# Kernel tuning notes

Hardware: AMD Instinct MI355X
Metric: run time of the kernel (lower is better)

The kernel has to match this reference:

```python
import jax, jax.numpy as jnp
import numpy as np

B, L, D, V, C = 16384, 50, 128, 91718, 11
H, HD, F = 4, 32, 6
NP = F * (F - 1) // 2  # 15 pairs
CIN = F * D + NP * D   # 2688


def setup_inputs() -> dict:
    key = jax.random.key(0)
    ks = jax.random.split(key, 32)
    inp = {}
    inp['item_id'] = jax.random.randint(ks[0], (B,), 0, V)
    inp['item_mm'] = jax.random.normal(ks[1], (B, D), dtype=jnp.float32)
    inp['likes'] = jax.random.randint(ks[2], (B,), 0, C)
    inp['views'] = jax.random.randint(ks[3], (B,), 0, C)
    inp['item_seq'] = jax.random.randint(ks[4], (B, L), 0, V)
    g = lambda k, shape, s: (jax.random.normal(k, shape, dtype=jnp.float32) * s)
    inp['item_emb'] = g(ks[5], (V, D), 0.02).at[0].set(0.0)  # padding_idx=0
    inp['cate_emb'] = g(ks[6], (C, D), 0.02)
    inp['mm_w'] = g(ks[7], (D, D), (2.0 / D) ** 0.5)
    inp['mm_b'] = jnp.zeros((D,), jnp.float32)
    inp['ln_g'] = jnp.ones((D,), jnp.float32)
    inp['ln_b'] = jnp.zeros((D,), jnp.float32)
    inp['gnn_W'] = g(ks[8], (H, D, HD), (2.0 / (D + HD)) ** 0.5 * 1.414)
    inp['gnn_a'] = g(ks[9], (H, 2 * HD, 1), 0.1)
    inp['se_w1'] = g(ks[10], (F, F // 2), 0.4)
    inp['se_b1'] = jnp.zeros((F // 2,), jnp.float32)
    inp['se_w2'] = g(ks[11], (F // 2, F), 0.4)
    inp['se_b2'] = jnp.zeros((F,), jnp.float32)
    inp['bi_W'] = g(ks[12], (F - 1, D, D), (2.0 / (2 * D)) ** 0.5)
    inp['mlp_w1'] = g(ks[13], (CIN, 512), (2.0 / CIN) ** 0.5)
    inp['mlp_b1'] = jnp.zeros((512,), jnp.float32)
    inp['bn1_g'] = jnp.ones((512,), jnp.float32)
    inp['bn1_b'] = jnp.zeros((512,), jnp.float32)
    inp['mlp_w2'] = g(ks[14], (512, 256), (2.0 / 512) ** 0.5)
    inp['mlp_b2'] = jnp.zeros((256,), jnp.float32)
    inp['bn2_g'] = jnp.ones((256,), jnp.float32)
    inp['bn2_b'] = jnp.zeros((256,), jnp.float32)
    inp['mlp_w3'] = g(ks[15], (256, 1), (2.0 / 256) ** 0.5)
    inp['mlp_b3'] = jnp.zeros((1,), jnp.float32)
    return inp


def _forward(item_id, item_mm, likes, views, item_seq,
             item_emb, cate_emb, mm_w, mm_b, ln_g, ln_b,
             gnn_W, gnn_a, se_w1, se_b1, se_w2, se_b2, bi_W,
             mlp_w1, mlp_b1, bn1_g, bn1_b, mlp_w2, mlp_b2, bn2_g, bn2_b,
             mlp_w3, mlp_b3):
    bsz = item_id.shape[0]
    eps = 1e-5

    user_feat = jnp.zeros((bsz, D), item_mm.dtype)
    like_feat = cate_emb[likes]
    view_feat = cate_emb[views]
    id_feat = item_emb[item_id]

    # mm_proj: Linear -> LayerNorm -> GELU (exact)
    y = item_mm @ mm_w + mm_b
    mu = y.mean(-1, keepdims=True)
    var = y.var(-1, keepdims=True)
    y = (y - mu) * jax.lax.rsqrt(var + eps) * ln_g + ln_b
    img_feat = jax.nn.gelu(y, approximate=False)

    # masked mean pooling of history
    seq_emb = item_emb[item_seq]                          # [B,L,D]
    mask = item_seq == 0
    seq_emb = jnp.where(mask[..., None], 0.0, seq_emb)
    cnt = jnp.clip(jnp.sum((~mask).astype(seq_emb.dtype), axis=1, keepdims=True), 1.0)
    hist_feat = seq_emb.sum(1) / cnt

    x = jnp.stack([user_feat, like_feat, view_feat, id_feat, img_feat, hist_feat], axis=1)  # [B,6,D]

    # GAT over 6-node fully-connected feature graph
    hp = jnp.einsum('bni,hio->bnho', x, gnn_W)            # [B,6,H,HD]
    a1 = gnn_a[:, :HD, 0]                                  # [H,HD]
    a2 = gnn_a[:, HD:, 0]
    ei = jnp.einsum('bnhd,hd->bhn', hp, a1)
    ej = jnp.einsum('bnhd,hd->bhn', hp, a2)
    e = ei[:, :, :, None] + ej[:, :, None, :]             # [B,H,6,6]
    e = jnp.where(e > 0, e, 0.2 * e)                       # LeakyReLU(0.2)
    att = jax.nn.softmax(e, axis=-1)                       # dropout off (eval)
    h_new = jnp.einsum('bhnm,bmho->bnho', att, hp).reshape(bsz, F, D)
    gnn_feat = jax.nn.elu(h_new + x)                       # in_dim == out_dim

    # SENet
    z = gnn_feat.mean(-1)                                  # [B,6]
    w = jax.nn.sigmoid(jax.nn.relu(z @ se_w1 + se_b1) @ se_w2 + se_b2)
    s = gnn_feat * w[..., None]

    # Bilinear ('each'): vid_i = s_i @ W_i, pairs (i,j), j>i
    vid = jnp.einsum('bfd,fde->bfe', s[:, :F - 1], bi_W)   # [B,5,D]
    p = jnp.stack([vid[:, i] * s[:, j] for i in range(F - 1) for j in range(i + 1, F)], axis=1)  # [B,15,D]

    c = jnp.concatenate([gnn_feat.reshape(bsz, -1), p.reshape(bsz, -1)], axis=1)  # [B,2688]

    # MLP with eval-mode BatchNorm (running mean 0, var 1) and dropout off
    bn = lambda t, g_, b_: t * (g_ / jnp.sqrt(1.0 + eps)) + b_
    h1 = jax.nn.gelu(bn(c @ mlp_w1 + mlp_b1, bn1_g, bn1_b), approximate=False)
    h2 = jax.nn.gelu(bn(h1 @ mlp_w2 + mlp_b2, bn2_g, bn2_b), approximate=False)
    out = jax.nn.sigmoid(h2 @ mlp_w3 + mlp_b3)
    return out.squeeze(-1)


def reference(item_id, item_mm, likes, views, item_seq,
              item_emb, cate_emb, mm_w, mm_b, ln_g, ln_b,
              gnn_W, gnn_a, se_w1, se_b1, se_w2, se_b2, bi_W,
              mlp_w1, mlp_b1, bn1_g, bn1_b, mlp_w2, mlp_b2, bn2_g, bn2_b,
              mlp_w3, mlp_b3):
    return _forward(item_id, item_mm, likes, views, item_seq,
                    item_emb, cate_emb, mm_w, mm_b, ln_g, ln_b,
                    gnn_W, gnn_a, se_w1, se_b1, se_w2, se_b2, bi_W,
                    mlp_w1, mlp_b1, bn1_g, bn1_b, mlp_w2, mlp_b2, bn2_g, bn2_b,
                    mlp_w3, mlp_b3)
```

## Files before the change

kernel.cpp:

```cpp
#include <hip/hip_runtime.h>
#include <hip/hip_bf16.h>
#include <cstdint>
#include <cstddef>

#define BB 16384

typedef float  floatx4 __attribute__((ext_vector_type(4)));
typedef float  floatx2 __attribute__((ext_vector_type(2)));
typedef __bf16 bf16x8  __attribute__((ext_vector_type(8)));

__device__ __forceinline__ unsigned short f2bf(float f) {
  union { float f; unsigned int u; } v; v.f = f;
  unsigned int r = v.u + 0x7FFFu + ((v.u >> 16) & 1u);
  return (unsigned short)(r >> 16);
}
__device__ __forceinline__ float bf2f(unsigned short h) {
  union { unsigned int u; float f; } v; v.u = ((unsigned int)h) << 16;
  return v.f;
}
__device__ __forceinline__ float gelu_exact(float x) {
  return 0.5f * x * (1.0f + erff(x * 0.7071067811865475f));
}
__device__ __forceinline__ void fp8x8_to_f32(uint2 v, float* o) {
  floatx2 p0 = __builtin_amdgcn_cvt_pk_f32_fp8((int)v.x, false);
  floatx2 p1 = __builtin_amdgcn_cvt_pk_f32_fp8((int)v.x, true);
  floatx2 p2 = __builtin_amdgcn_cvt_pk_f32_fp8((int)v.y, false);
  floatx2 p3 = __builtin_amdgcn_cvt_pk_f32_fp8((int)v.y, true);
  o[0] = p0.x; o[1] = p0.y; o[2] = p1.x; o[3] = p1.y;
  o[4] = p2.x; o[5] = p2.y; o[6] = p3.x; o[7] = p3.y;
}

#define ALOAD16(g, l) \
  __builtin_amdgcn_global_load_lds((const __attribute__((address_space(1))) void*)(g), \
                                   (__attribute__((address_space(3))) void*)(l), 16, 0, 0)

__global__ __launch_bounds__(256)
void k_prep(const float* __restrict__ gnn_W, const float* __restrict__ gnn_a,
            const float* __restrict__ item_mm, const float* __restrict__ item_emb,
            const float* __restrict__ w1, const float* __restrict__ w2,
            const float* __restrict__ bi_W, const float* __restrict__ mm_w,
            unsigned short* __restrict__ wallt2, unsigned short* __restrict__ immb,
            unsigned char* __restrict__ iembf8,
            unsigned short* __restrict__ w1t, unsigned short* __restrict__ w2t,
            unsigned short* __restrict__ biwt, unsigned short* __restrict__ mmwt)
{
  __shared__ float tile[64][65];
  if (blockIdx.x < 2048) {
    const int total = 18432 + 524288 + 1467488;
    for (int id = blockIdx.x * 256 + threadIdx.x; id < total; id += 2048 * 256) {
      if (id < 18432) {
        int n = id / 128, k = id % 128;
        if (n < 128) {
          wallt2[id] = f2bf(gnn_W[(n >> 5) * 4096 + k * 32 + (n & 31)]);
        } else if (n < 136) {
          int h = (n - 128) & 3;
          int off = (n < 132) ? 0 : 32;
          float s = 0.f;
          for (int o = 0; o < 32; o++)
            s += gnn_W[h * 4096 + k * 32 + o] * gnn_a[h * 64 + off + o];
          wallt2[id] = f2bf(s);
        } else {
          wallt2[id] = 0;
        }
      } else if (id < 542720) {
        int l = id - 18432;
        float4 v = ((const float4*)item_mm)[l];
        ushort4 o; o.x = f2bf(v.x); o.y = f2bf(v.y); o.z = f2bf(v.z); o.w = f2bf(v.w);
        ((ushort4*)immb)[l] = o;
      } else {
        int l = id - 542720;
        const float4 v0 = ((const float4*)item_emb)[l * 2];
        const float4 v1 = ((const float4*)item_emb)[l * 2 + 1];
        int lo = __builtin_amdgcn_cvt_pk_fp8_f32(v0.x, v0.y, 0, false);
        lo     = __builtin_amdgcn_cvt_pk_fp8_f32(v0.z, v0.w, lo, true);
        int hi = __builtin_amdgcn_cvt_pk_fp8_f32(v1.x, v1.y, 0, false);
        hi     = __builtin_amdgcn_cvt_pk_fp8_f32(v1.z, v1.w, hi, true);
        uint2 o; o.x = (unsigned int)lo; o.y = (unsigned int)hi;
        ((uint2*)iembf8)[l] = o;
      }
    }
  } else {
    int blk = blockIdx.x - 2048;
    const float* in; unsigned short* outp; int R, C, bx, by;
    if (blk < 336)      { in = w1; outp = w1t; R = 2688; C = 512; bx = blk % 8; by = blk / 8; }
    else if (blk < 368) { blk -= 336; in = w2; outp = w2t; R = 512; C = 256; bx = blk % 4; by = blk / 4; }
    else if (blk < 388) { blk -= 368; int f = blk / 4; int r2 = blk % 4;
                          in = bi_W + f * 16384; outp = biwt + f * 16384;
                          R = 128; C = 128; bx = r2 % 2; by = r2 / 2; }
    else                { blk -= 388; in = mm_w; outp = mmwt; R = 128; C = 128;
                          bx = blk % 2; by = blk / 2; }
    const int c0 = bx * 64, r0 = by * 64;
    const int lr = threadIdx.x >> 6;
    const int lc = threadIdx.x & 63;
    #pragma unroll
    for (int i = 0; i < 16; i++) {
      int r = lr + i * 4;
      tile[r][lc] = in[(size_t)(r0 + r) * C + c0 + lc];
    }
    __syncthreads();
    #pragma unroll
    for (int i = 0; i < 16; i++) {
      int c = lr + i * 4;
      outp[(size_t)(c0 + c) * R + r0 + lc] = f2bf(tile[lc][c]);
    }
  }
}

__global__ __launch_bounds__(512)
void k_featmm(const int* __restrict__ item_id, const int* __restrict__ likes,
              const int* __restrict__ views, const int* __restrict__ item_seq,
              const unsigned char* __restrict__ iembf8, const float* __restrict__ cate_emb,
              const unsigned short* __restrict__ immb, const unsigned short* __restrict__ mmwt,
              const float* __restrict__ mm_b, const float* __restrict__ ln_g,
              const float* __restrict__ ln_b, unsigned short* __restrict__ xb)
{
  __shared__ __align__(16) char smem[64 * 130 * 4];
  const int t = threadIdx.x, lane = t & 63, w = t >> 6;

  if (blockIdx.x < 2048) {
    const int b = blockIdx.x * 8 + w;
    const int g = lane >> 4, l16 = lane & 15;
    const size_t base = (size_t)b * 768;
    const int li = likes[b], vi = views[b], id = item_id[b];

    const int ng = (g < 2) ? 13 : 12;
    int idxs[13];
    #pragma unroll
    for (int e = 0; e < 13; e++)
      idxs[e] = (e < ng) ? item_seq[b * 50 + g + 4 * e] : 0;

    float acc[8] = {0.f, 0.f, 0.f, 0.f, 0.f, 0.f, 0.f, 0.f};
    float cnt = 0.f;
    #pragma unroll
    for (int e = 0; e < 13; e++) {
      const int idx = idxs[e];
      if (idx != 0) {
        cnt += 1.0f;
        uint2 v = *(const uint2*)&iembf8[(size_t)idx * 128 + l16 * 8];
        float dv[8];
        fp8x8_to_f32(v, dv);
        #pragma unroll
        for (int k = 0; k < 8; k++) acc[k] += dv[k];
      }
    }
    #pragma unroll
    for (int k = 0; k < 8; k++) {
      acc[k] += __shfl_xor(acc[k], 16, 64);
      acc[k] += __shfl_xor(acc[k], 32, 64);
    }
    cnt += __shfl_xor(cnt, 16, 64);
    cnt += __shfl_xor(cnt, 32, 64);
    const float ic = 1.0f / fmaxf(cnt, 1.0f);

    *(unsigned int*)&xb[base + lane * 2] = 0u;

    if (g == 0) {
      uint4 o;
      o.x = (unsigned int)f2bf(acc[0] * ic) | ((unsigned int)f2bf(acc[1] * ic) << 16);
      o.y = (unsigned int)f2bf(acc[2] * ic) | ((unsigned int)f2bf(acc[3] * ic) << 16);
      o.z = (unsigned int)f2bf(acc[4] * ic) | ((unsigned int)f2bf(acc[5] * ic) << 16);
      o.w = (unsigned int)f2bf(acc[6] * ic) | ((unsigned int)f2bf(acc[7] * ic) << 16);
      *(uint4*)&xb[base + 640 + l16 * 8] = o;
    } else if (g == 1) {
      uint2 v = *(const uint2*)&iembf8[(size_t)id * 128 + l16 * 8];
      float dv[8];
      fp8x8_to_f32(v, dv);
      uint4 o;
      o.x = (unsigned int)f2bf(dv[0]) | ((unsigned int)f2bf(dv[1]) << 16);
      o.y = (unsigned int)f2bf(dv[2]) | ((unsigned int)f2bf(dv[3]) << 16);
      o.z = (unsigned int)f2bf(dv[4]) | ((unsigned int)f2bf(dv[5]) << 16);
      o.w = (unsigned int)f2bf(dv[6]) | ((unsigned int)f2bf(dv[7]) << 16);
      *(uint4*)&xb[base + 384 + l16 * 8] = o;
    } else {
      const int ci = (g == 2) ? li : vi;
      const float4 v0 = *(const float4*)&cate_emb[(size_t)ci * 128 + l16 * 8];
      const float4 v1 = *(const float4*)&cate_emb[(size_t)ci * 128 + l16 * 8 + 4];
      uint4 o;
      o.x = (unsigned int)f2bf(v0.x) | ((unsigned int)f2bf(v0.y) << 16);
      o.y = (unsigned int)f2bf(v0.z) | ((unsigned int)f2bf(v0.w) << 16);
      o.z = (unsigned int)f2bf(v1.x) | ((unsigned int)f2bf(v1.y) << 16);
      o.w = (unsigned int)f2bf(v1.z) | ((unsigned int)f2bf(v1.w) << 16);
      *(uint4*)&xb[base + 128 + (g - 2) * 128 + l16 * 8] = o;
    }
    return;
  }

  unsigned short* As = (unsigned short*)smem;
  unsigned short* Bs = (unsigned short*)(smem + 8192);
  float* cls = (float*)smem;

  const int lr = lane & 15, lq = lane >> 4;
  const int m0 = (blockIdx.x - 2048) * 64;

  floatx4 acc[4];
  #pragma unroll
  for (int a = 0; a < 4; a++) acc[a] = (floatx4){0.f, 0.f, 0.f, 0.f};

  const int srow = lane >> 3;
  const int schk = (lane & 7) ^ srow;
  const int rb0 = w * 24;

  for (int k0 = 0; k0 < 128; k0 += 64) {
    __syncthreads();
    #pragma unroll
    for (int q = 0; q < 3; q++) {
      const int rb = rb0 + q * 8;
      if (rb < 64) ALOAD16(immb + (size_t)(m0 + rb + srow) * 128 + k0 + schk * 8, As + rb * 64);
      else { const int rbb = rb - 64; ALOAD16(mmwt + (size_t)(rbb + srow) * 128 + k0 + schk * 8, Bs + rbb * 64); }
    }
    __syncthreads();
    #pragma unroll
    for (int ko = 0; ko < 2; ko++) {
      bf16x8 af[4], bv;
      #pragma unroll
      for (int mt = 0; mt < 4; mt++) {
        const int row = mt * 16 + lr;
        const int pc = (ko * 4 + lq) ^ (lr & 7);
        af[mt] = __builtin_bit_cast(bf16x8, *(const uint4*)&As[row * 64 + pc * 8]);
      }
      {
        const int row = w * 16 + lr;
        const int pc = (ko * 4 + lq) ^ (lr & 7);
        bv = __builtin_bit_cast(bf16x8, *(const uint4*)&Bs[row * 64 + pc * 8]);
      }
      #pragma unroll
      for (int mt = 0; mt < 4; mt++)
        acc[mt] = __builtin_amdgcn_mfma_f32_16x16x32_bf16(af[mt], bv, acc[mt], 0, 0, 0);
    }
  }

  __syncthreads();
  #pragma unroll
  for (int mt = 0; mt < 4; mt++)
    #pragma unroll
    for (int i = 0; i < 4; i++) {
      const int rr = mt * 16 + lq * 4 + i;
      const int cc = w * 16 + lr;
      cls[rr * 130 + cc] = acc[mt][i] + mm_b[cc];
    }
  __syncthreads();

  const float2 g2 = *(const float2*)&ln_g[lane * 2];
  const float2 b2 = *(const float2*)&ln_b[lane * 2];
  #pragma unroll
  for (int rr = 0; rr < 8; rr++) {
    const int r = w * 8 + rr;
    float2 v = *(const float2*)&cls[r * 130 + lane * 2];
    float s = v.x + v.y, s2 = v.x * v.x + v.y * v.y;
    #pragma unroll
    for (int o = 32; o > 0; o >>= 1) { s += __shfl_xor(s, o, 64); s2 += __shfl_xor(s2, o, 64); }
    float mu  = s * (1.0f / 128.0f);
    float var = s2 * (1.0f / 128.0f) - mu * mu;
    float rs  = rsqrtf(var + 1e-5f);
    float t0 = gelu_exact((v.x - mu) * rs * g2.x + b2.x);
    float t1 = gelu_exact((v.y - mu) * rs * g2.y + b2.y);
    unsigned int pk = (unsigned int)f2bf(t0) | ((unsigned int)f2bf(t1) << 16);
    *(unsigned int*)&xb[(size_t)(m0 + r) * 768 + 512 + lane * 2] = pk;
  }
}

__global__ __launch_bounds__(512)
void gemm_mlp1(const unsigned short* __restrict__ A, const unsigned short* __restrict__ Bt,
               unsigned short* __restrict__ Cp,
               const float* __restrict__ bias, const float* __restrict__ bng,
               const float* __restrict__ bnb)
{
  int p = blockIdx.y * gridDim.x + blockIdx.x;
  int xcd = p & 7, slot = p >> 3;
  const int bx = slot % gridDim.x;
  const int by = xcd * (gridDim.y >> 3) + slot / gridDim.x;
  const int n0 = bx * 128;
  const int m0 = by * 128;

  __shared__ __align__(16) unsigned short lds[2 * 16384];
  const int t = threadIdx.x, lane = t & 63, w = t >> 6;
  const int wm = w & 1, wn = w >> 1;
  const int lr = lane & 15, lq = lane >> 4;

  floatx4 acc[4][2];
  #pragma unroll
  for (int a = 0; a < 4; a++)
    #pragma unroll
    for (int b = 0; b < 2; b++) acc[a][b] = (floatx4){0.f, 0.f, 0.f, 0.f};

  const int srow = lane >> 3;
  const int schk = (lane & 7) ^ srow;
  const int rb0 = w * 32;

  auto STAGE = [&](int k0, int s) {
    unsigned short* Ad = lds + s * 16384;
    unsigned short* Bd = Ad + 8192;
    #pragma unroll
    for (int q = 0; q < 4; q++) {
      const int rb = rb0 + q * 8;
      if (rb < 128) {
        ALOAD16(A + (size_t)(m0 + rb + srow) * 2688 + k0 + schk * 8, Ad + rb * 64);
      } else {
        ALOAD16(Bt + (size_t)(n0 + rb - 128 + srow) * 2688 + k0 + schk * 8, Bd + (rb - 128) * 64);
      }
    }
  };

  STAGE(0, 0);
  __syncthreads();

  for (int kt = 0; kt < 42; kt++) {
    const int cur = kt & 1;
    if (kt < 41) STAGE((kt + 1) * 64, cur ^ 1);
    const unsigned short* As = lds + cur * 16384;
    const unsigned short* Bs = As + 8192;
    #pragma unroll
    for (int ko = 0; ko < 2; ko++) {
      bf16x8 af[4], bfv[2];
      #pragma unroll
      for (int mt = 0; mt < 4; mt++) {
        const int row = wm * 64 + mt * 16 + lr;
        const int pc = (ko * 4 + lq) ^ (lr & 7);
        af[mt] = __builtin_bit_cast(bf16x8, *(const uint4*)&As[row * 64 + pc * 8]);
      }
      #pragma unroll
      for (int nt = 0; nt < 2; nt++) {
        const int row = wn * 32 + nt * 16 + lr;
        const int pc = (ko * 4 + lq) ^ (lr & 7);
        bfv[nt] = __builtin_bit_cast(bf16x8, *(const uint4*)&Bs[row * 64 + pc * 8]);
      }
      #pragma unroll
      for (int mt = 0; mt < 4; mt++)
        #pragma unroll
        for (int nt = 0; nt < 2; nt++)
          acc[mt][nt] = __builtin_amdgcn_mfma_f32_16x16x32_bf16(af[mt], bfv[nt], acc[mt][nt], 0, 0, 0);
    }
    __syncthreads();
  }

  #pragma unroll
  for (int mt = 0; mt < 4; mt++)
    #pragma unroll
    for (int nt = 0; nt < 2; nt++)
      #pragma unroll
      for (int i = 0; i < 4; i++) {
        const int cm = m0 + wm * 64 + mt * 16 + lq * 4 + i;
        const int cn = n0 + wn * 32 + nt * 16 + lr;
        float tt = acc[mt][nt][i] + bias[cn];
        tt = tt * (bng[cn] * 0.9999950000374997f) + bnb[cn];
        Cp[(size_t)cm * 512 + cn] = f2bf(gelu_exact(tt));
      }
}

__global__ __launch_bounds__(256)
void k_hpatt(const unsigned short* __restrict__ xb, const unsigned short* __restrict__ wallt2,
             const float* __restrict__ se_w1, const float* __restrict__ se_b1,
             const float* __restrict__ se_w2, const float* __restrict__ se_b2,
             unsigned short* __restrict__ c, unsigned short* __restrict__ sb)
{
  __shared__ __align__(16) char smem[30720];
  unsigned short* As = (unsigned short*)smem;
  unsigned short* Bs = (unsigned short*)(smem + 12288);
  unsigned short* hps = (unsigned short*)smem;

  const int t = threadIdx.x, lane = t & 63, w = t >> 6;
  const int wm = w & 1, wn = w >> 1;
  const int lr = lane & 15, lq = lane >> 4;
  const int m0 = blockIdx.x * 96;

  floatx4 acc[3][5];
  #pragma unroll
  for (int a = 0; a < 3; a++)
    #pragma unroll
    for (int b = 0; b < 5; b++) acc[a][b] = (floatx4){0.f, 0.f, 0.f, 0.f};

  const int srow = lane >> 3;
  const int schk = (lane & 7) ^ srow;

  for (int k0 = 0; k0 < 128; k0 += 64) {
    __syncthreads();
    #pragma unroll
    for (int q = 0; q < 8; q++) {
      const int e = w + 4 * q;
      if (e < 30) {
        const int rb = e * 8;
        if (rb < 96) {
          ALOAD16(xb + (size_t)(m0 + rb + srow) * 128 + k0 + schk * 8, As + rb * 64);
        } else {
          const int rbb = rb - 96;
          ALOAD16(wallt2 + (size_t)(rbb + srow) * 128 + k0 + schk * 8, Bs + rbb * 64);
        }
      }
    }
    __syncthreads();
    #pragma unroll
    for (int ko = 0; ko < 2; ko++) {
      bf16x8 af[3];
      #pragma unroll
      for (int mt = 0; mt < 3; mt++) {
        const int row = wm * 48 + mt * 16 + lr;
        const int pc = (ko * 4 + lq) ^ (lr & 7);
        af[mt] = __builtin_bit_cast(bf16x8, *(const uint4*)&As[row * 64 + pc * 8]);
      }
      #pragma unroll
      for (int nt = 0; nt < 5; nt++) {
        if (nt < 4 || wn == 0) {
          const int tid = wn + 2 * nt;
          const int row = tid * 16 + lr;
          const int pc = (ko * 4 + lq) ^ (lr & 7);
          bf16x8 bfv = __builtin_bit_cast(bf16x8, *(const uint4*)&Bs[row * 64 + pc * 8]);
          #pragma unroll
          for (int mt = 0; mt < 3; mt++)
            acc[mt][nt] = __builtin_amdgcn_mfma_f32_16x16x32_bf16(af[mt], bfv, acc[mt][nt], 0, 0, 0);
        }
      }
    }
  }

  __syncthreads();
  #pragma unroll
  for (int mt = 0; mt < 3; mt++)
    #pragma unroll
    for (int nt = 0; nt < 5; nt++)
      if (nt < 4 || wn == 0) {
        const int tid = wn + 2 * nt;
        #pragma unroll
        for (int i = 0; i < 4; i++) {
          const int rr = wm * 48 + mt * 16 + lq * 4 + i;
          const int cc = tid * 16 + lr;
          hps[rr * 146 + cc] = f2bf(acc[mt][nt][i]);
        }
      }
  __syncthreads();

  const int hh = lane >> 4;

  for (int it = 0; it < 4; it++) {
    const int lb = w * 4 + it;
    const int b = blockIdx.x * 16 + lb;
    const unsigned short* hb = hps + lb * 6 * 146;

    float2 vm[6];
    float ein[6], ejn[6];
    #pragma unroll
    for (int m = 0; m < 6; m++) {
      unsigned int pk = *(const unsigned int*)&hb[m * 146 + lane * 2];
      vm[m].x = bf2f((unsigned short)(pk & 0xFFFFu));
      vm[m].y = bf2f((unsigned short)(pk >> 16));
      ein[m] = bf2f(hb[m * 146 + 128 + hh]);
      ejn[m] = bf2f(hb[m * 146 + 132 + hh]);
    }

    float g0[6], g1[6], zz[6];
    #pragma unroll
    for (int n = 0; n < 6; n++) {
      float ev[6]; float mx = -1e30f;
      #pragma unroll
      for (int m = 0; m < 6; m++) {
        float e = ein[n] + ejn[m];
        e = e > 0.f ? e : 0.2f * e;
        ev[m] = e; mx = fmaxf(mx, e);
      }
      float ss = 0.f;
      #pragma unroll
      for (int m = 0; m < 6; m++) { ev[m] = __expf(ev[m] - mx); ss += ev[m]; }
      const float inv = 1.0f / ss;
      float hn0 = 0.f, hn1 = 0.f;
      #pragma unroll
      for (int m = 0; m < 6; m++) {
        const float a = ev[m] * inv;
        hn0 += a * vm[m].x; hn1 += a * vm[m].y;
      }
      unsigned int xp = *(const unsigned int*)&xb[(size_t)b * 768 + n * 128 + lane * 2];
      float A0 = hn0 + bf2f((unsigned short)(xp & 0xFFFFu));
      float A1 = hn1 + bf2f((unsigned short)(xp >> 16));
      A0 = A0 > 0.f ? A0 : __expf(A0) - 1.0f;
      A1 = A1 > 0.f ? A1 : __expf(A1) - 1.0f;
      g0[n] = A0; g1[n] = A1;
      float zacc = A0 + A1;
      #pragma unroll
      for (int o = 32; o > 0; o >>= 1) zacc += __shfl_xor(zacc, o, 64);
      zz[n] = zacc * (1.0f / 128.0f);
    }

    float rr3[3];
    #pragma unroll
    for (int j = 0; j < 3; j++) {
      float a = se_b1[j];
      #pragma unroll
      for (int n = 0; n < 6; n++) a += zz[n] * se_w1[n * 3 + j];
      rr3[j] = fmaxf(a, 0.f);
    }
    float wse[6];
    #pragma unroll
    for (int n = 0; n < 6; n++) {
      float a = se_b2[n];
      #pragma unroll
      for (int j = 0; j < 3; j++) a += rr3[j] * se_w2[j * 6 + n];
      wse[n] = 1.0f / (1.0f + __expf(-a));
    }

    #pragma unroll
    for (int n = 0; n < 6; n++) {
      unsigned int pc = (unsigned int)f2bf(g0[n]) | ((unsigned int)f2bf(g1[n]) << 16);
      unsigned int ps = (unsigned int)f2bf(g0[n] * wse[n]) | ((unsigned int)f2bf(g1[n] * wse[n]) << 16);
      *(unsigned int*)&c[(size_t)b * 2688 + n * 128 + lane * 2]  = pc;
      *(unsigned int*)&sb[(size_t)b * 768 + n * 128 + lane * 2]  = ps;
    }
  }
}

__global__ __launch_bounds__(256)
void gemm_vid(const unsigned short* __restrict__ sbb, const unsigned short* __restrict__ biwt,
              unsigned short* __restrict__ c)
{
  const int z = blockIdx.z;
  const int m0 = blockIdx.y * 128;
  __shared__ __align__(16) unsigned short smem[2 * 16384];
  const int t = threadIdx.x;
  const int lane = t & 63, w = t >> 6;
  const int wm = w & 1, wn = w >> 1;
  const int lr = lane & 15, lq = lane >> 4;

  floatx4 acc[4][4];
  #pragma unroll
  for (int a = 0; a < 4; a++)
    #pragma unroll
    for (int b = 0; b < 4; b++) acc[a][b] = (floatx4){0.f, 0.f, 0.f, 0.f};

  const int srow = lane >> 3;
  const int schk = (lane & 7) ^ srow;
  const unsigned short* Ag = sbb + (size_t)(m0 + w * 32 + srow) * 768 + z * 128 + schk * 8;
  const unsigned short* Bg = biwt + z * 16384 + (size_t)(w * 32 + srow) * 128 + schk * 8;

  auto STAGE = [&](int k0, int s) {
    unsigned short* AsW = smem + s * 16384 + w * 32 * 64;
    unsigned short* BsW = smem + s * 16384 + 8192 + w * 32 * 64;
    #pragma unroll
    for (int q = 0; q < 4; q++) {
      ALOAD16(Ag + k0 + (size_t)(q * 8) * 768, AsW + q * 512);
      ALOAD16(Bg + k0 + (size_t)(q * 8) * 128, BsW + q * 512);
    }
  };

  STAGE(0, 0);
  __syncthreads();

  #pragma unroll
  for (int kt = 0; kt < 2; kt++) {
    if (kt == 0) STAGE(64, 1);
    const unsigned short* As = smem + (kt ? 16384 : 0);
    const unsigned short* Bs = As + 8192;
    #pragma unroll
    for (int ko = 0; ko < 2; ko++) {
      bf16x8 af[4], bfv[4];
      #pragma unroll
      for (int mt = 0; mt < 4; mt++) {
        const int row = wm * 64 + mt * 16 + lr;
        const int pc = (ko * 4 + lq) ^ (lr & 7);
        af[mt] = __builtin_bit_cast(bf16x8, *(const uint4*)&As[row * 64 + pc * 8]);
      }
      #pragma unroll
      for (int nt = 0; nt < 4; nt++) {
        const int row = wn * 64 + nt * 16 + lr;
        const int pc = (ko * 4 + lq) ^ (lr & 7);
        bfv[nt] = __builtin_bit_cast(bf16x8, *(const uint4*)&Bs[row * 64 + pc * 8]);
      }
      #pragma unroll
      for (int mt = 0; mt < 4; mt++)
        #pragma unroll
        for (int nt = 0; nt < 4; nt++)
          acc[mt][nt] = __builtin_amdgcn_mfma_f32_16x16x32_bf16(af[mt], bfv[nt], acc[mt][nt], 0, 0, 0);
    }
    __syncthreads();
  }

  #pragma unroll
  for (int mt = 0; mt < 4; mt++)
    #pragma unroll
    for (int nt = 0; nt < 4; nt++)
      #pragma unroll
      for (int i = 0; i < 4; i++) {
        const int rr = wm * 64 + mt * 16 + lq * 4 + i;
        const int cc = wn * 64 + nt * 16 + lr;
        smem[rr * 130 + cc] = f2bf(acc[mt][nt][i]);
      }
  __syncthreads();

  const int pb0[5] = {0, 5, 9, 12, 14};
  const int npairs = 5 - z;
  const int tot = 128 * 32 * npairs;
  for (int e = t; e < tot; e += 256) {
    const int g  = e & 31;
    const int rp = e >> 5;
    const int p  = rp % npairs;
    const int r  = rp / npairs;
    ushort4 vv = *(const ushort4*)&smem[r * 130 + g * 4];
    ushort4 sv = *(const ushort4*)&sbb[(size_t)(m0 + r) * 768 + (z + 1 + p) * 128 + g * 4];
    ushort4 o;
    o.x = f2bf(bf2f(vv.x) * bf2f(sv.x));
    o.y = f2bf(bf2f(vv.y) * bf2f(sv.y));
    o.z = f2bf(bf2f(vv.z) * bf2f(sv.z));
    o.w = f2bf(bf2f(vv.w) * bf2f(sv.w));
    *(ushort4*)&c[(size_t)(m0 + r) * 2688 + 768 + (size_t)(pb0[z] + p) * 128 + g * 4] = o;
  }
}

__global__ __launch_bounds__(512)
void k_mlp2out(const unsigned short* __restrict__ A, const unsigned short* __restrict__ Bt,
               const float* __restrict__ b2v, const float* __restrict__ bng,
               const float* __restrict__ bnb, const float* __restrict__ w3,
               const float* __restrict__ b3, float* __restrict__ out)
{
  __shared__ __align__(16) char smem[81920];
  unsigned short* h2s = (unsigned short*)smem;

  const int t = threadIdx.x, lane = t & 63, w = t >> 6;
  const int lr = lane & 15, lq = lane >> 4;
  const int m0 = blockIdx.x * 64;

  floatx4 acc[4][2];
  #pragma unroll
  for (int a = 0; a < 4; a++)
    #pragma unroll
    for (int b = 0; b < 2; b++) acc[a][b] = (floatx4){0.f, 0.f, 0.f, 0.f};

  const int srow = lane >> 3;
  const int schk = (lane & 7) ^ srow;
  const int rb0 = w * 40;

  auto STAGE = [&](int k0, int s) {
    unsigned short* As_ = (unsigned short*)smem + s * 20480;
    unsigned short* Bs_ = As_ + 4096;
    #pragma unroll
    for (int q = 0; q < 5; q++) {
      const int rb = rb0 + q * 8;
      if (rb < 64) ALOAD16(A + (size_t)(m0 + rb + srow) * 512 + k0 + schk * 8, As_ + rb * 64);
      else { const int rbb = rb - 64; ALOAD16(Bt + (size_t)(rbb + srow) * 512 + k0 + schk * 8, Bs_ + rbb * 64); }
    }
  };

  STAGE(0, 0);
  __syncthreads();

  for (int kt = 0; kt < 8; kt++) {
    const int cur = kt & 1;
    if (kt < 7) STAGE((kt + 1) * 64, cur ^ 1);
    const unsigned short* As = (const unsigned short*)smem + cur * 20480;
    const unsigned short* Bs = As + 4096;
    #pragma unroll
    for (int ko = 0; ko < 2; ko++) {
      bf16x8 af[4], bfv[2];
      #pragma unroll
      for (int mt = 0; mt < 4; mt++) {
        const int row = mt * 16 + lr;
        const int pc = (ko * 4 + lq) ^ (lr & 7);
        af[mt] = __builtin_bit_cast(bf16x8, *(const uint4*)&As[row * 64 + pc * 8]);
      }
      #pragma unroll
      for (int nt = 0; nt < 2; nt++) {
        const int row = w * 32 + nt * 16 + lr;
        const int pc = (ko * 4 + lq) ^ (lr & 7);
        bfv[nt] = __builtin_bit_cast(bf16x8, *(const uint4*)&Bs[row * 64 + pc * 8]);
      }
      #pragma unroll
      for (int mt = 0; mt < 4; mt++)
        #pragma unroll
        for (int nt = 0; nt < 2; nt++)
          acc[mt][nt] = __builtin_amdgcn_mfma_f32_16x16x32_bf16(af[mt], bfv[nt], acc[mt][nt], 0, 0, 0);
    }
    __syncthreads();
  }

  #pragma unroll
  for (int mt = 0; mt < 4; mt++)
    #pragma unroll
    for (int nt = 0; nt < 2; nt++)
      #pragma unroll
      for (int i = 0; i < 4; i++) {
        const int rr = mt * 16 + lq * 4 + i;
        const int cc = w * 32 + nt * 16 + lr;
        float tt = acc[mt][nt][i] + b2v[cc];
        tt = tt * (bng[cc] * 0.9999950000374997f) + bnb[cc];
        h2s[rr * 264 + cc] = f2bf(gelu_exact(tt));
      }
  __syncthreads();

  const float4 w4 = *(const float4*)&w3[lane * 4];
  #pragma unroll
  for (int rr = 0; rr < 8; rr++) {
    const int r = w * 8 + rr;
    ushort4 v = *(const ushort4*)&h2s[r * 264 + lane * 4];
    float a = bf2f(v.x) * w4.x + bf2f(v.y) * w4.y + bf2f(v.z) * w4.z + bf2f(v.w) * w4.w;
    #pragma unroll
    for (int o = 32; o > 0; o >>= 1) a += __shfl_xor(a, o, 64);
    if (lane == 0) out[m0 + r] = 1.0f / (1.0f + __expf(-(a + b3[0])));
  }
}

#define OFF_MMWT   0ull
#define OFF_BIWT   65536ull
#define OFF_W1T    229376ull
#define OFF_W2T    2981888ull
#define OFF_IMMB   3244032ull
#define OFF_XB     7438336ull
#define OFF_SB     57769984ull
#define OFF_C      82935808ull
#define OFF_IEMB   179404800ull
#define OFF_WALLT2 191144704ull

extern "C" void kernel_launch(void* const* d_in, const int* in_sizes, int n_in,
                              void* d_out, int out_size, void* d_ws, size_t ws_size,
                              hipStream_t stream)
{
  const int*   item_id  = (const int*)  d_in[0];
  const float* item_mm  = (const float*)d_in[1];
  const int*   likes    = (const int*)  d_in[2];
  const int*   views    = (const int*)  d_in[3];
  const int*   item_seq = (const int*)  d_in[4];
  const float* item_emb = (const float*)d_in[5];
  const float* cate_emb = (const float*)d_in[6];
  const float* mm_w     = (const float*)d_in[7];
  const float* mm_b     = (const float*)d_in[8];
  const float* ln_g     = (const float*)d_in[9];
  const float* ln_b     = (const float*)d_in[10];
  const float* gnn_W    = (const float*)d_in[11];
  const float* gnn_a    = (const float*)d_in[12];
  const float* se_w1    = (const float*)d_in[13];
  const float* se_b1    = (const float*)d_in[14];
  const float* se_w2    = (const float*)d_in[15];
  const float* se_b2    = (const float*)d_in[16];
  const float* bi_W     = (const float*)d_in[17];
  const float* mlp_w1   = (const float*)d_in[18];
  const float* mlp_b1   = (const float*)d_in[19];
  const float* bn1_g    = (const float*)d_in[20];
  const float* bn1_b    = (const float*)d_in[21];
  const float* mlp_w2   = (const float*)d_in[22];
  const float* mlp_b2   = (const float*)d_in[23];
  const float* bn2_g    = (const float*)d_in[24];
  const float* bn2_b    = (const float*)d_in[25];
  const float* mlp_w3   = (const float*)d_in[26];
  const float* mlp_b3   = (const float*)d_in[27];
  float* out = (float*)d_out;

  char* ws = (char*)d_ws;
  unsigned short* mmwt   = (unsigned short*)(ws + OFF_MMWT);
  unsigned short* biwt   = (unsigned short*)(ws + OFF_BIWT);
  unsigned short* w1t    = (unsigned short*)(ws + OFF_W1T);
  unsigned short* w2t    = (unsigned short*)(ws + OFF_W2T);
  unsigned short* immb   = (unsigned short*)(ws + OFF_IMMB);
  unsigned short* xb     = (unsigned short*)(ws + OFF_XB);
  unsigned short* sbb    = (unsigned short*)(ws + OFF_SB);
  unsigned short* cbuf   = (unsigned short*)(ws + OFF_C);
  unsigned short* h1b    = (unsigned short*)(ws + OFF_XB);
  unsigned char*  iembf8 = (unsigned char*) (ws + OFF_IEMB);
  unsigned short* wallt2 = (unsigned short*)(ws + OFF_WALLT2);

  k_prep<<<2440, 256, 0, stream>>>(gnn_W, gnn_a, item_mm, item_emb,
                                   mlp_w1, mlp_w2, bi_W, mm_w,
                                   wallt2, immb, iembf8, w1t, w2t, biwt, mmwt);
  k_featmm<<<2304, 512, 0, stream>>>(item_id, likes, views, item_seq, iembf8, cate_emb,
                                     immb, mmwt, mm_b, ln_g, ln_b, xb);
  k_hpatt<<<1024, 256, 0, stream>>>(xb, wallt2, se_w1, se_b1, se_w2, se_b2, cbuf, sbb);
  gemm_vid<<<dim3(1, 128, 5), 256, 0, stream>>>(sbb, biwt, cbuf);
  gemm_mlp1<<<dim3(4, 128), 512, 0, stream>>>(cbuf, w1t, h1b, mlp_b1, bn1_g, bn1_b);
  k_mlp2out<<<256, 512, 0, stream>>>(h1b, w2t, mlp_b2, bn2_g, bn2_b, mlp_w3, mlp_b3, out);
}
```

Before: 315.5 us.

## Fuse bilinear vid GEMM and pair products into attention kernel

Removes the separate gemm_vid kernel and its sb global buffer. The SE-weighted features are now written into shared memory inside k_hpatt, and each block runs the per-field bilinear projections with MFMA, multiplies by the partner fields and writes the pair products straight into c. This cuts one kernel launch and a global write/read round trip of the weighted features. In exchange, bi_W tiles are reloaded from global memory per block without LDS staging, and the final stores are scalar 2-byte writes, which may coalesce less well.

```diff
diff --git a/kernel.cpp b/kernel.cpp
--- a/kernel.cpp
+++ b/kernel.cpp
@@ -351,7 +351,8 @@
 void k_hpatt(const unsigned short* __restrict__ xb, const unsigned short* __restrict__ wallt2,
              const float* __restrict__ se_w1, const float* __restrict__ se_b1,
              const float* __restrict__ se_w2, const float* __restrict__ se_b2,
-             unsigned short* __restrict__ c, unsigned short* __restrict__ sb)
+             const unsigned short* __restrict__ biwt,
+             unsigned short* __restrict__ c)
 {
   __shared__ __align__(16) char smem[30720];
   unsigned short* As = (unsigned short*)smem;
@@ -433,7 +434,7 @@
   for (int it = 0; it < 4; it++) {
     const int lb = w * 4 + it;
     const int b = blockIdx.x * 16 + lb;
-    const unsigned short* hb = hps + lb * 6 * 146;
+    unsigned short* hb = hps + lb * 6 * 146;
 
     float2 vm[6];
     float ein[6], ejn[6];
@@ -499,105 +500,52 @@
     for (int n = 0; n < 6; n++) {
       unsigned int pc = (unsigned int)f2bf(g0[n]) | ((unsigned int)f2bf(g1[n]) << 16);
       unsigned int ps = (unsigned int)f2bf(g0[n] * wse[n]) | ((unsigned int)f2bf(g1[n] * wse[n]) << 16);
-      *(unsigned int*)&c[(size_t)b * 2688 + n * 128 + lane * 2]  = pc;
-      *(unsigned int*)&sb[(size_t)b * 768 + n * 128 + lane * 2]  = ps;
-    }
-  }
-}
-
-__global__ __launch_bounds__(256)
-void gemm_vid(const unsigned short* __restrict__ sbb, const unsigned short* __restrict__ biwt,
-              unsigned short* __restrict__ c)
-{
-  const int z = blockIdx.z;
-  const int m0 = blockIdx.y * 128;
-  __shared__ __align__(16) unsigned short smem[2 * 16384];
-  const int t = threadIdx.x;
-  const int lane = t & 63, w = t >> 6;
-  const int wm = w & 1, wn = w >> 1;
-  const int lr = lane & 15, lq = lane >> 4;
-
-  floatx4 acc[4][4];
-  #pragma unroll
-  for (int a = 0; a < 4; a++)
-    #pragma unroll
-    for (int b = 0; b < 4; b++) acc[a][b] = (floatx4){0.f, 0.f, 0.f, 0.f};
-
-  const int srow = lane >> 3;
-  const int schk = (lane & 7) ^ srow;
-  const unsigned short* Ag = sbb + (size_t)(m0 + w * 32 + srow) * 768 + z * 128 + schk * 8;
-  const unsigned short* Bg = biwt + z * 16384 + (size_t)(w * 32 + srow) * 128 + schk * 8;
-
-  auto STAGE = [&](int k0, int s) {
-    unsigned short* AsW = smem + s * 16384 + w * 32 * 64;
-    unsigned short* BsW = smem + s * 16384 + 8192 + w * 32 * 64;
-    #pragma unroll
-    for (int q = 0; q < 4; q++) {
-      ALOAD16(Ag + k0 + (size_t)(q * 8) * 768, AsW + q * 512);
-      ALOAD16(Bg + k0 + (size_t)(q * 8) * 128, BsW + q * 512);
-    }
-  };
-
-  STAGE(0, 0);
+      *(unsigned int*)&c[(size_t)b * 2688 + n * 128 + lane * 2] = pc;
+      *(unsigned int*)&hb[n * 146 + lane * 2] = ps;
+    }
+  }
+
   __syncthreads();
-
-  #pragma unroll
-  for (int kt = 0; kt < 2; kt++) {
-    if (kt == 0) STAGE(64, 1);
-    const unsigned short* As = smem + (kt ? 16384 : 0);
-    const unsigned short* Bs = As + 8192;
-    #pragma unroll
-    for (int ko = 0; ko < 2; ko++) {
-      bf16x8 af[4], bfv[4];
-      #pragma unroll
-      for (int mt = 0; mt < 4; mt++) {
-        const int row = wm * 64 + mt * 16 + lr;
-        const int pc = (ko * 4 + lq) ^ (lr & 7);
-        af[mt] = __builtin_bit_cast(bf16x8, *(const uint4*)&As[row * 64 + pc * 8]);
-      }
-      #pragma unroll
-      for (int nt = 0; nt < 4; nt++) {
-        const int row = wn * 64 + nt * 16 + lr;
-        const int pc = (ko * 4 + lq) ^ (lr & 7);
-        bfv[nt] = __builtin_bit_cast(bf16x8, *(const uint4*)&Bs[row * 64 + pc * 8]);
-      }
-      #pragma unroll
-      for (int mt = 0; mt < 4; mt++)
+  {
+    const size_t B0 = (size_t)blockIdx.x * 16;
+    for (int z = 0; z < 5; z++) {
+      floatx4 vacc[2];
+      vacc[0] = (floatx4){0.f, 0.f, 0.f, 0.f};
+      vacc[1] = (floatx4){0.f, 0.f, 0.f, 0.f};
+      #pragma unroll
+      for (int kk = 0; kk < 4; kk++) {
+        const int abase = (lr * 6 + z) * 146 + kk * 32 + lq * 8;
+        uint4 au;
+        au.x = *(const unsigned int*)&hps[abase + 0];
+        au.y = *(const unsigned int*)&hps[abase + 2];
+        au.z = *(const unsigned int*)&hps[abase + 4];
+        au.w = *(const unsigned int*)&hps[abase + 6];
+        const bf16x8 af = __builtin_bit_cast(bf16x8, au);
         #pragma unroll
-        for (int nt = 0; nt < 4; nt++)
-          acc[mt][nt] = __builtin_amdgcn_mfma_f32_16x16x32_bf16(af[mt], bfv[nt], acc[mt][nt], 0, 0, 0);
-    }
-    __syncthreads();
-  }
-
-  #pragma unroll
-  for (int mt = 0; mt < 4; mt++)
-    #pragma unroll
-    for (int nt = 0; nt < 4; nt++)
-      #pragma unroll
-      for (int i = 0; i < 4; i++) {
-        const int rr = wm * 64 + mt * 16 + lq * 4 + i;
-        const int cc = wn * 64 + nt * 16 + lr;
-        smem[rr * 130 + cc] = f2bf(acc[mt][nt][i]);
-      }
-  __syncthreads();
-
-  const int pb0[5] = {0, 5, 9, 12, 14};
-  const int npairs = 5 - z;
-  const int tot = 128 * 32 * npairs;
-  for (int e = t; e < tot; e += 256) {
-    const int g  = e & 31;
-    const int rp = e >> 5;
-    const int p  = rp % npairs;
-    const int r  = rp / npairs;
-    ushort4 vv = *(const ushort4*)&smem[r * 130 + g * 4];
-    ushort4 sv = *(const ushort4*)&sbb[(size_t)(m0 + r) * 768 + (z + 1 + p) * 128 + g * 4];
-    ushort4 o;
-    o.x = f2bf(bf2f(vv.x) * bf2f(sv.x));
-    o.y = f2bf(bf2f(vv.y) * bf2f(sv.y));
-    o.z = f2bf(bf2f(vv.z) * bf2f(sv.z));
-    o.w = f2bf(bf2f(vv.w) * bf2f(sv.w));
-    *(ushort4*)&c[(size_t)(m0 + r) * 2688 + 768 + (size_t)(pb0[z] + p) * 128 + g * 4] = o;
+        for (int nt = 0; nt < 2; nt++) {
+          const int col = (w + nt * 4) * 16 + lr;
+          const bf16x8 bv = __builtin_bit_cast(bf16x8,
+            *(const uint4*)&biwt[z * 16384 + col * 128 + kk * 32 + lq * 8]);
+          vacc[nt] = __builtin_amdgcn_mfma_f32_16x16x32_bf16(af, bv, vacc[nt], 0, 0, 0);
+        }
+      }
+      const int npairs = 5 - z;
+      const int pbz = z * (11 - z) / 2;
+      #pragma unroll
+      for (int nt = 0; nt < 2; nt++) {
+        const int cc = (w + nt * 4) * 16 + lr;
+        #pragma unroll
+        for (int i = 0; i < 4; i++) {
+          const int r = lq * 4 + i;
+          const float vv = bf2f(f2bf(vacc[nt][i]));
+          for (int p = 0; p < npairs; p++) {
+            const int j = z + 1 + p;
+            const float sv = bf2f(hps[(r * 6 + j) * 146 + cc]);
+            c[(B0 + r) * 2688 + 768 + (size_t)(pbz + p) * 128 + cc] = f2bf(vv * sv);
+          }
+        }
+      }
+    }
   }
 }
 
@@ -745,7 +693,6 @@
   unsigned short* w2t    = (unsigned short*)(ws + OFF_W2T);
   unsigned short* immb   = (unsigned short*)(ws + OFF_IMMB);
   unsigned short* xb     = (unsigned short*)(ws + OFF_XB);
-  unsigned short* sbb    = (unsigned short*)(ws + OFF_SB);
   unsigned short* cbuf   = (unsigned short*)(ws + OFF_C);
   unsigned short* h1b    = (unsigned short*)(ws + OFF_XB);
   unsigned char*  iembf8 = (unsigned char*) (ws + OFF_IEMB);
@@ -756,8 +703,8 @@
                                    wallt2, immb, iembf8, w1t, w2t, biwt, mmwt);
   k_featmm<<<2304, 512, 0, stream>>>(item_id, likes, views, item_seq, iembf8, cate_emb,
                                      immb, mmwt, mm_b, ln_g, ln_b, xb);
-  k_hpatt<<<1024, 256, 0, stream>>>(xb, wallt2, se_w1, se_b1, se_w2, se_b2, cbuf, sbb);
-  gemm_vid<<<dim3(1, 128, 5), 256, 0, stream>>>(sbb, biwt, cbuf);
+  k_hpatt<<<1024, 256, 0, stream>>>(xb, wallt2, se_w1, se_b1, se_w2, se_b2,
+                                    biwt, cbuf);
   gemm_mlp1<<<dim3(4, 128), 512, 0, stream>>>(cbuf, w1t, h1b, mlp_b1, bn1_g, bn1_b);
   k_mlp2out<<<256, 512, 0, stream>>>(h1b, w2t, mlp_b2, bn2_g, bn2_b, mlp_w3, mlp_b3, out);
 }
```

After: 300.7 us. 1.05x faster.
